# Kernel tuning notes

Measured on AMD Instinct MI355X. Metric: run time of the kernel, lower is better.

## Reference

```python
import jax, jax.numpy as jnp
import numpy as np

N_NODES = 100000
N_EDGES = 1600000
IN_FEAT = 128
UNITS = 64


def setup_inputs() -> dict:
    key = jax.random.key(0)
    k1, k2, k3, k4, k5 = jax.random.split(key, 5)
    node_states = jax.random.normal(k1, (N_NODES, IN_FEAT), dtype=jnp.float32)
    # edges[:,0] is the destination/segment id; the original TF code's
    # repeat(bincount) normalization assumes edges sorted by edges[:,0].
    dst = jnp.sort(jax.random.randint(k2, (N_EDGES,), 0, N_NODES))
    src = jax.random.randint(k3, (N_EDGES,), 0, N_NODES)
    edges = jnp.stack([dst, src], axis=1).astype(jnp.int64)
    kernel = jax.random.normal(k4, (IN_FEAT, UNITS), dtype=jnp.float32) * 0.05
    kernel_attention = jax.random.normal(k5, (2 * UNITS, 1), dtype=jnp.float32) * 0.05
    return {"node_states": node_states, "edges": edges,
            "kernel": kernel, "kernel_attention": kernel_attention}


def reference(node_states, edges, kernel, kernel_attention):
    n_nodes = node_states.shape[0]
    dst = edges[:, 0]  # segment ids (aggregation target)
    src = edges[:, 1]  # neighbor being gathered

    h = node_states @ kernel                      # [N, U]
    h_dst = h[dst]                                # [E, U]
    h_src = h[src]                                # [E, U]
    # concat(h_dst, h_src) @ a  ==  h_dst @ a[:U] + h_src @ a[U:]
    u = kernel_attention.shape[0] // 2
    scores = (h_dst @ kernel_attention[:u] + h_src @ kernel_attention[u:])[:, 0]  # [E]
    scores = jax.nn.leaky_relu(scores, negative_slope=0.2)  # tf default alpha=0.2
    scores = jnp.exp(jnp.clip(scores, -2.0, 2.0))

    score_sum = jax.ops.segment_sum(scores, dst, num_segments=n_nodes)  # [N]
    attn = scores / score_sum[dst]                                      # [E]

    out = jax.ops.segment_sum(h_src * attn[:, None], dst, num_segments=n_nodes)  # [N, U]
    return out
```

## Files before the change

kernel.cpp:

```cpp
#include <hip/hip_runtime.h>
#include <hip/hip_bf16.h>

#define NN 100000
#define NE 1600000
#define NF 128
#define UU 64

typedef __attribute__((ext_vector_type(8))) short short8;
typedef __attribute__((ext_vector_type(4))) float f32x4;

static const size_t OFF_FLAG = 0;
static const size_t OFF_SRC  = 256;
static const size_t OFF_H2   = OFF_SRC + (size_t)NE * 4;
static const size_t OFF_AD   = OFF_H2  + (size_t)NN * UU * 2;
static const size_t OFF_AS   = OFF_AD  + (size_t)NN * 4;
static const size_t OFF_ROW  = OFF_AS  + (size_t)NN * 4;
static const size_t OFF_WP   = OFF_ROW + (size_t)(NN + 1) * 4;

__device__ __forceinline__ unsigned short bfr(float v) {
    unsigned u = __float_as_uint(v);
    return (unsigned short)((u + 0x7FFFu + ((u >> 16) & 1u)) >> 16);
}

__global__ __launch_bounds__(256) void prep(const int* __restrict__ ew,
                                            const float* __restrict__ W,
                                            int* __restrict__ flag,
                                            unsigned short* __restrict__ Wp) {
    if (threadIdx.x == 0) {
        int a = ew[2 * 400000 + 1] | ew[2 * 800000 + 1] |
                ew[2 * 1200000 + 1] | ew[2 * 1599999 + 1];
        *flag = (a == 0) ? 1 : 0;
    }
    for (int i = threadIdx.x; i < 8192; i += 256) {
        int j   = i & 7;
        int l15 = (i >> 3) & 15;
        int quad = (i >> 7) & 3;
        int kb  = (i >> 9) & 3;
        int nt  = i >> 11;
        Wp[i] = bfr(W[(size_t)(kb * 32 + quad * 8 + j) * UU + nt * 16 + l15]);
    }
}

#define GEMM_BLOCKS   1563
#define ROWS_BLOCKS   391
#define UNPACK_BLOCKS 1563

__global__ __launch_bounds__(256) void mega(const float* __restrict__ X,
                                            const void* __restrict__ edges,
                                            const int* __restrict__ flag,
                                            const unsigned short* __restrict__ Wp,
                                            const float* __restrict__ ka,
                                            unsigned short* __restrict__ h2,
                                            float* __restrict__ a_dst,
                                            float* __restrict__ a_src,
                                            int* __restrict__ src32,
                                            int* __restrict__ rows) {
    int bid = blockIdx.x;
    int tid = threadIdx.x;

    if (bid < GEMM_BLOCKS) {
        int wv = tid >> 6, lane = tid & 63;
        int quad = lane >> 4, l15 = lane & 15;
        int nb = bid * 64 + wv * 16;
        int row = nb + l15; if (row >= NN) row = NN - 1;
        const float* xr = X + (size_t)row * NF + quad * 8;

        short8 afrag[4];
#pragma unroll
        for (int kb = 0; kb < 4; kb++) {
            float4 p0 = *(const float4*)(xr + kb * 32);
            float4 p1 = *(const float4*)(xr + kb * 32 + 4);
            short8 a;
            a[0] = (short)bfr(p0.x); a[1] = (short)bfr(p0.y);
            a[2] = (short)bfr(p0.z); a[3] = (short)bfr(p0.w);
            a[4] = (short)bfr(p1.x); a[5] = (short)bfr(p1.y);
            a[6] = (short)bfr(p1.z); a[7] = (short)bfr(p1.w);
            afrag[kb] = a;
        }

        f32x4 acc[4] = {f32x4{0,0,0,0}, f32x4{0,0,0,0}, f32x4{0,0,0,0}, f32x4{0,0,0,0}};
        const short8* wpf = (const short8*)Wp;
#pragma unroll
        for (int nt = 0; nt < 4; nt++) {
#pragma unroll
            for (int kb = 0; kb < 4; kb++) {
                short8 b = wpf[((nt * 4 + kb) * 4 + quad) * 16 + l15];
                acc[nt] = __builtin_amdgcn_mfma_f32_16x16x32_bf16(afrag[kb], b, acc[nt], 0, 0, 0);
            }
        }

        float kad[4], kas[4];
#pragma unroll
        for (int nt = 0; nt < 4; nt++) {
            kad[nt] = ka[nt * 16 + l15];
            kas[nt] = ka[64 + nt * 16 + l15];
        }
#pragma unroll
        for (int r = 0; r < 4; r++) {
            int m = nb + quad * 4 + r;
            if (m < NN) {
#pragma unroll
                for (int nt = 0; nt < 4; nt++)
                    h2[(size_t)m * UU + nt * 16 + l15] = bfr(acc[nt][r]);
            }
            float pd = acc[0][r] * kad[0] + acc[1][r] * kad[1] + acc[2][r] * kad[2] + acc[3][r] * kad[3];
            float ps = acc[0][r] * kas[0] + acc[1][r] * kas[1] + acc[2][r] * kas[2] + acc[3][r] * kas[3];
            pd += __shfl_xor(pd, 1); pd += __shfl_xor(pd, 2);
            pd += __shfl_xor(pd, 4); pd += __shfl_xor(pd, 8);
            ps += __shfl_xor(ps, 1); ps += __shfl_xor(ps, 2);
            ps += __shfl_xor(ps, 4); ps += __shfl_xor(ps, 8);
            if (l15 == 0 && m < NN) { a_dst[m] = pd; a_src[m] = ps; }
        }
        return;
    }
    bid -= GEMM_BLOCKS;

    if (bid < ROWS_BLOCKS) {
        int n = bid * 256 + tid;
        if (n > NN) return;
        if (n == NN) { rows[NN] = NE; return; }
        int fl = *flag;
        const int* ew = (const int*)edges;
        int lo = 0, hi = NE;
        while (lo < hi) {
            int mid = (lo + hi) >> 1;
            int d = fl ? ew[4 * (size_t)mid] : ew[2 * (size_t)mid];
            if (d < n) lo = mid + 1; else hi = mid;
        }
        rows[n] = lo;
        return;
    }
    bid -= ROWS_BLOCKS;

    {
        int fl = *flag;
        const int* ew = (const int*)edges;
#pragma unroll
        for (int t = 0; t < 4; t++) {
            int i = bid * 1024 + t * 256 + tid;
            if (i < NE) src32[i] = fl ? ew[4 * (size_t)i + 2] : ew[2 * (size_t)i + 1];
        }
    }
}

__device__ __forceinline__ float edge_score(float ad, float as) {
    float sc = ad + as;
    sc = sc > 0.f ? sc : 0.2f * sc;
    sc = fminf(fmaxf(sc, -2.f), 2.f);
    return __expf(sc);
}

__global__ __launch_bounds__(256) void aggregate(const int* __restrict__ rows,
                                                 const int* __restrict__ srcv,
                                                 const unsigned short* __restrict__ h2,
                                                 const float* __restrict__ a_dst,
                                                 const float* __restrict__ a_src,
                                                 float* __restrict__ out) {
    int gid = blockIdx.x * blockDim.x + threadIdx.x;
    int n = gid >> 6;
    int lane = gid & 63;
    if (n >= NN) return;
    int s = rows[n], e = rows[n + 1];
    int cnt = e - s;
    float ad = a_dst[n];
    int g = lane >> 4, gl = lane & 15;
    float4 acc = make_float4(0.f, 0.f, 0.f, 0.f);

    if (cnt <= 64) {
        int idx = s + lane;
        int mysrc = 0; float myscore = 0.f;
        if (idx < e) { mysrc = srcv[idx]; myscore = edge_score(ad, a_src[mysrc]); }
        float t = myscore;
#pragma unroll
        for (int off = 32; off; off >>= 1) t += __shfl_xor(t, off);
        float inv = (cnt > 0) ? 1.f / t : 0.f;
        for (int c = 0; c < cnt; c += 4) {
            int j = c + g;
            float wj = __shfl(myscore, j) * inv;
            int sj = __shfl(mysrc, j);
            uint2 r = *(const uint2*)(h2 + (size_t)sj * UU + gl * 4);
            acc.x += wj * __uint_as_float(r.x << 16);
            acc.y += wj * __uint_as_float(r.x & 0xFFFF0000u);
            acc.z += wj * __uint_as_float(r.y << 16);
            acc.w += wj * __uint_as_float(r.y & 0xFFFF0000u);
        }
    } else {
        float ssum = 0.f;
        for (int i = s + lane; i < e; i += 64) ssum += edge_score(ad, a_src[srcv[i]]);
#pragma unroll
        for (int off = 32; off; off >>= 1) ssum += __shfl_xor(ssum, off);
        float inv = 1.f / ssum;
        for (int c = s; c < e; c += 64) {
            int i = c + lane;
            int mysrc = 0; float myscore = 0.f;
            if (i < e) { mysrc = srcv[i]; myscore = edge_score(ad, a_src[mysrc]); }
            int lim = min(64, e - c);
            for (int c2 = 0; c2 < lim; c2 += 4) {
                int j = c2 + g;
                float wj = __shfl(myscore, j) * inv;
                int sj = __shfl(mysrc, j);
                uint2 r = *(const uint2*)(h2 + (size_t)sj * UU + gl * 4);
                acc.x += wj * __uint_as_float(r.x << 16);
                acc.y += wj * __uint_as_float(r.x & 0xFFFF0000u);
                acc.z += wj * __uint_as_float(r.y << 16);
                acc.w += wj * __uint_as_float(r.y & 0xFFFF0000u);
            }
        }
    }
    acc.x += __shfl_xor(acc.x, 32); acc.y += __shfl_xor(acc.y, 32);
    acc.z += __shfl_xor(acc.z, 32); acc.w += __shfl_xor(acc.w, 32);
    acc.x += __shfl_xor(acc.x, 16); acc.y += __shfl_xor(acc.y, 16);
    acc.z += __shfl_xor(acc.z, 16); acc.w += __shfl_xor(acc.w, 16);
    if (lane < 16) *(float4*)(out + (size_t)n * UU + gl * 4) = acc;
}

extern "C" void kernel_launch(void* const* d_in, const int* in_sizes, int n_in,
                              void* d_out, int out_size, void* d_ws, size_t ws_size,
                              hipStream_t stream) {
    const float* X  = (const float*)d_in[0];
    const void*  Ed = d_in[1];
    const float* W  = (const float*)d_in[2];
    const float* KA = (const float*)d_in[3];
    float* out = (float*)d_out;

    char* ws = (char*)d_ws;
    int*            flag  = (int*)(ws + OFF_FLAG);
    int*            src32 = (int*)(ws + OFF_SRC);
    unsigned short* h2    = (unsigned short*)(ws + OFF_H2);
    float*          a_dst = (float*)(ws + OFF_AD);
    float*          a_src = (float*)(ws + OFF_AS);
    int*            rows  = (int*)(ws + OFF_ROW);
    unsigned short* Wp    = (unsigned short*)(ws + OFF_WP);

    prep<<<1, 256, 0, stream>>>((const int*)Ed, W, flag, Wp);
    mega<<<GEMM_BLOCKS + ROWS_BLOCKS + UNPACK_BLOCKS, 256, 0, stream>>>(
        X, Ed, flag, Wp, KA, h2, a_dst, a_src, src32, rows);
    aggregate<<<(NN * 64 + 255) / 256, 256, 0, stream>>>(rows, src32, h2, a_dst, a_src, out);
}
```

Baseline: 166.6 us.

## Widen aggregate gathers to 16-byte loads, batch edges, defer normalization

The aggregate kernel now assigns 8 lanes per source row, each loading 16 bytes of bf16, so each wave processes 8 edges at once instead of 4. Four loads are issued before any accumulation so memory requests overlap, and the per-edge division by the score sum is replaced by one scale after the reduction. The src-extraction prep step also switches to 16-byte vector loads of the edge array. In exchange the wave holds more registers and does wasted gathers on padded zero-score edges, since batches always cover 32 edges.

```diff
diff --git a/kernel.cpp b/kernel.cpp
--- a/kernel.cpp
+++ b/kernel.cpp
@@ -134,11 +134,24 @@
 
     {
         int fl = *flag;
-        const int* ew = (const int*)edges;
-#pragma unroll
-        for (int t = 0; t < 4; t++) {
-            int i = bid * 1024 + t * 256 + tid;
-            if (i < NE) src32[i] = fl ? ew[4 * (size_t)i + 2] : ew[2 * (size_t)i + 1];
+        if (fl) {
+            const int4* ev = (const int4*)edges;
+#pragma unroll
+            for (int t = 0; t < 4; t++) {
+                int i = bid * 1024 + t * 256 + tid;
+                if (i < NE) { int4 v = ev[i]; src32[i] = v.z; }
+            }
+        } else {
+            const int4* ev = (const int4*)edges;
+#pragma unroll
+            for (int t = 0; t < 2; t++) {
+                int p = bid * 512 + t * 256 + tid;
+                if (p * 2 < NE) {
+                    int4 v = ev[p];
+                    int2 st = make_int2(v.y, v.w);
+                    *(int2*)(src32 + p * 2) = st;
+                }
+            }
         }
     }
 }
@@ -163,55 +176,73 @@
     int s = rows[n], e = rows[n + 1];
     int cnt = e - s;
     float ad = a_dst[n];
-    int g = lane >> 4, gl = lane & 15;
-    float4 acc = make_float4(0.f, 0.f, 0.f, 0.f);
+    int g = lane >> 3, gl = lane & 7;
+    const unsigned short* h2g = h2 + gl * 8;
+    float acc[8] = {0.f, 0.f, 0.f, 0.f, 0.f, 0.f, 0.f, 0.f};
+    float inv;
+
+#define BATCH4(C0, SCORE, SRC)                                                   \
+    {                                                                            \
+        uint4 rr[4]; float sw[4];                                                \
+        _Pragma("unroll")                                                        \
+        for (int t = 0; t < 4; t++) {                                            \
+            int j = ((C0) + t) * 8 + g;                                          \
+            int sj = __shfl((SRC), j);                                           \
+            sw[t] = __shfl((SCORE), j);                                          \
+            rr[t] = *(const uint4*)(h2g + (size_t)sj * UU);                      \
+        }                                                                        \
+        _Pragma("unroll")                                                        \
+        for (int t = 0; t < 4; t++) {                                            \
+            acc[0] += sw[t] * __uint_as_float(rr[t].x << 16);                    \
+            acc[1] += sw[t] * __uint_as_float(rr[t].x & 0xFFFF0000u);            \
+            acc[2] += sw[t] * __uint_as_float(rr[t].y << 16);                    \
+            acc[3] += sw[t] * __uint_as_float(rr[t].y & 0xFFFF0000u);            \
+            acc[4] += sw[t] * __uint_as_float(rr[t].z << 16);                    \
+            acc[5] += sw[t] * __uint_as_float(rr[t].z & 0xFFFF0000u);            \
+            acc[6] += sw[t] * __uint_as_float(rr[t].w << 16);                    \
+            acc[7] += sw[t] * __uint_as_float(rr[t].w & 0xFFFF0000u);            \
+        }                                                                        \
+    }
 
     if (cnt <= 64) {
         int idx = s + lane;
         int mysrc = 0; float myscore = 0.f;
         if (idx < e) { mysrc = srcv[idx]; myscore = edge_score(ad, a_src[mysrc]); }
+        int nb = (cnt + 31) >> 5;
+        for (int b = 0; b < nb; b++) BATCH4(b * 4, myscore, mysrc);
         float t = myscore;
 #pragma unroll
         for (int off = 32; off; off >>= 1) t += __shfl_xor(t, off);
-        float inv = (cnt > 0) ? 1.f / t : 0.f;
-        for (int c = 0; c < cnt; c += 4) {
-            int j = c + g;
-            float wj = __shfl(myscore, j) * inv;
-            int sj = __shfl(mysrc, j);
-            uint2 r = *(const uint2*)(h2 + (size_t)sj * UU + gl * 4);
-            acc.x += wj * __uint_as_float(r.x << 16);
-            acc.y += wj * __uint_as_float(r.x & 0xFFFF0000u);
-            acc.z += wj * __uint_as_float(r.y << 16);
-            acc.w += wj * __uint_as_float(r.y & 0xFFFF0000u);
-        }
+        inv = (cnt > 0) ? 1.f / t : 0.f;
     } else {
         float ssum = 0.f;
         for (int i = s + lane; i < e; i += 64) ssum += edge_score(ad, a_src[srcv[i]]);
 #pragma unroll
         for (int off = 32; off; off >>= 1) ssum += __shfl_xor(ssum, off);
-        float inv = 1.f / ssum;
+        inv = 1.f / ssum;
         for (int c = s; c < e; c += 64) {
             int i = c + lane;
             int mysrc = 0; float myscore = 0.f;
             if (i < e) { mysrc = srcv[i]; myscore = edge_score(ad, a_src[mysrc]); }
-            int lim = min(64, e - c);
-            for (int c2 = 0; c2 < lim; c2 += 4) {
-                int j = c2 + g;
-                float wj = __shfl(myscore, j) * inv;
-                int sj = __shfl(mysrc, j);
-                uint2 r = *(const uint2*)(h2 + (size_t)sj * UU + gl * 4);
-                acc.x += wj * __uint_as_float(r.x << 16);
-                acc.y += wj * __uint_as_float(r.x & 0xFFFF0000u);
-                acc.z += wj * __uint_as_float(r.y << 16);
-                acc.w += wj * __uint_as_float(r.y & 0xFFFF0000u);
-            }
-        }
-    }
-    acc.x += __shfl_xor(acc.x, 32); acc.y += __shfl_xor(acc.y, 32);
-    acc.z += __shfl_xor(acc.z, 32); acc.w += __shfl_xor(acc.w, 32);
-    acc.x += __shfl_xor(acc.x, 16); acc.y += __shfl_xor(acc.y, 16);
-    acc.z += __shfl_xor(acc.z, 16); acc.w += __shfl_xor(acc.w, 16);
-    if (lane < 16) *(float4*)(out + (size_t)n * UU + gl * 4) = acc;
+            BATCH4(0, myscore, mysrc);
+            BATCH4(4, myscore, mysrc);
+        }
+    }
+#undef BATCH4
+
+#pragma unroll
+    for (int i = 0; i < 8; i++) {
+        acc[i] += __shfl_xor(acc[i], 32);
+        acc[i] += __shfl_xor(acc[i], 16);
+        acc[i] += __shfl_xor(acc[i], 8);
+        acc[i] *= inv;
+    }
+    if (lane < 8) {
+        float4 o0 = make_float4(acc[0], acc[1], acc[2], acc[3]);
+        float4 o1 = make_float4(acc[4], acc[5], acc[6], acc[7]);
+        *(float4*)(out + (size_t)n * UU + lane * 8)     = o0;
+        *(float4*)(out + (size_t)n * UU + lane * 8 + 4) = o1;
+    }
 }
 
 extern "C" void kernel_launch(void* const* d_in, const int* in_sizes, int n_in,
```

Result: slower. 170.4 us (+2.3%).
